# Optimization experiments

Hardware: AMD Instinct MI355X
Metric: run time of the kernel (lower is better)

## Reference

```python
import jax, jax.numpy as jnp
import numpy as np
from jax import lax

UP = 4          # upscale_factor (pixel_shuffle factor hardcoded to 4 in ReconBlock)
OUT_CH = UP * UP * 5 * 5  # 400
MID_CH = UP * 5           # 20


def setup_inputs() -> dict:
    key = jax.random.key(0)
    ks = jax.random.split(key, 5)
    B, A, H, W = 2, 5, 96, 96
    pic = jax.random.uniform(ks[0], (B, A, A, H, W), dtype=jnp.float32)
    w1 = jax.random.normal(ks[1], (OUT_CH, 1, 5, 5, 9, 9), dtype=jnp.float32) * 0.02
    b1 = jnp.zeros((OUT_CH,), jnp.float32)
    w2a = jax.random.normal(ks[2], (MID_CH, 1, 3, 3, 5, 5), dtype=jnp.float32) * 0.02
    b2a = jnp.zeros((MID_CH,), jnp.float32)
    w2b = jax.random.normal(ks[3], (OUT_CH, MID_CH, 3, 3, 5, 5), dtype=jnp.float32) * 0.02
    b2b = jnp.zeros((OUT_CH,), jnp.float32)
    return {"pic": pic, "w1": w1, "b1": b1, "w2a": w2a, "b2a": b2a,
            "w2b": w2b, "b2b": b2b}


def _conv4d(x, w):
    # x: [B, Cin, A1, A2, H, W], w: [Cout, Cin, k1, k2, k3, k4], VALID, stride 1
    return lax.conv_general_dilated(x, w, window_strides=(1, 1, 1, 1),
                                    padding='VALID')


def _bias(b):
    return b[None, :, None, None, None, None]


def reference(pic, w1, b1, w2a, b2a, w2b, b2b):
    B, A1, A2, H, W = pic.shape
    # Padder: pad H,W by 4 each side with value 0.5
    padded = jnp.full((B, A1, A2, H + 8, W + 8), 0.5, dtype=pic.dtype)
    padded = padded.at[:, :, :, 4:-4, 4:-4].set(pic)
    x = padded[:, None]  # [B,1,A1,A2,H+8,W+8]

    # DimBlock_1: single 4D conv (5,5,9,9); ReLU defined but never applied
    p1 = _conv4d(x, w1) + _bias(b1)              # [B,400,1,1,H,W]

    # DimBlock_2: two 4D convs (3,3,5,5) with ReLU
    buf = jax.nn.relu(_conv4d(x, w2a) + _bias(b2a))   # [B,20,3,3,H+4,W+4]
    p2 = jax.nn.relu(_conv4d(buf, w2b) + _bias(b2b))  # [B,400,1,1,H,W]

    # BottleNeck
    mid = (p1 + p2) / 2                           # [B,400,1,1,H,W]

    # ReconBlock: take angular position (0,0), pixel_shuffle(4), split 25 -> 5x5
    y = mid[:, :, 0, 0]                           # [B,400,H,W]
    Bc, C, Hh, Ww = y.shape
    r = 4
    y = y.reshape(Bc, 25, r, r, Hh, Ww)
    y = y.transpose(0, 1, 4, 2, 5, 3).reshape(Bc, 25, Hh * r, Ww * r)
    return y.reshape(Bc, 5, 5, Hh * r, Ww * r)
```

## Files before the change

kernel.cpp:

```cpp
#include <hip/hip_runtime.h>
#include <hip/hip_bf16.h>


typedef __attribute__((ext_vector_type(8))) unsigned short ushort8;
typedef __attribute__((ext_vector_type(8))) __bf16 bf16x8;
typedef __attribute__((ext_vector_type(4))) float f32x4;

#define NB 2
#define HSLOT 576
#define WST 14336

static __device__ __forceinline__ unsigned short f2bf(float f) {
    __hip_bfloat16 h = __float2bfloat16(f);
    return *reinterpret_cast<unsigned short*>(&h);
}
static __device__ __forceinline__ float bf2f(unsigned short u) {
    unsigned int v = ((unsigned int)u) << 16;
    return __uint_as_float(v);
}
static __device__ __forceinline__ void gload16(const unsigned short* g, unsigned short* l) {
    __builtin_amdgcn_global_load_lds(
        (const __attribute__((address_space(1))) unsigned int*)(const void*)g,
        (__attribute__((address_space(3))) unsigned int*)(void*)l, 16, 0, 0);
}

__global__ __launch_bounds__(256) void pad_kernel(const float* __restrict__ pic,
                                                  unsigned short* __restrict__ Pn,
                                                  unsigned short* __restrict__ Pp) {
    int idx = blockIdx.x * 256 + threadIdx.x;
    if (idx >= NB * 104 * 104) return;
    int x = idx % 104;
    int y = (idx / 104) % 104;
    int b = idx / (104 * 104);
    unsigned short vals[32];
    bool inter = (y >= 4 && y < 100 && x >= 4 && x < 100);
#pragma unroll
    for (int c = 0; c < 25; ++c) {
        float v = inter ? pic[((b * 25 + c) * 96 + (y - 4)) * 96 + (x - 4)] : 0.5f;
        vals[c] = f2bf(v);
        Pp[((b * 25 + c) * 104 + y) * 104 + x] = vals[c];
    }
#pragma unroll
    for (int c = 25; c < 32; ++c) vals[c] = 0;
    ushort8* dst = (ushort8*)(Pn + idx * 32);
#pragma unroll
    for (int j = 0; j < 4; ++j) dst[j] = *(ushort8*)&vals[j * 8];
}

#define NWA (6 * 25 * 7 * 4 * 64 * 8)
#define NWB (81 * 7 * 4 * 64 * 8)
__global__ __launch_bounds__(256) void prep_w_kernel(const float* __restrict__ w2b,
                                                     const float* __restrict__ w1,
                                                     unsigned short* __restrict__ WpA,
                                                     unsigned short* __restrict__ WpB) {
    int idx = blockIdx.x * 256 + threadIdx.x;
    if (idx < NWA) {
        int e = idx & 7, lane = (idx >> 3) & 63, n = (idx >> 9) & 3;
        int r = idx >> 11;
        int ocb = r % 7; r /= 7;
        int tap = r % 25; int cc = r / 25;
        int oc = ocb * 64 + n * 16 + (lane & 15);
        int k  = cc * 32 + (lane >> 4) * 8 + e;
        float v = 0.f;
        if (oc < 400 && k < 180) {
            int mc = k % 20, uv = k / 20;
            v = w2b[oc * 4500 + (mc * 9 + uv) * 25 + tap];
        }
        WpA[idx] = f2bf(v);
    } else {
        int kx = idx - NWA;
        if (kx >= NWB) return;
        int e = kx & 7, lane = (kx >> 3) & 63, n = (kx >> 9) & 3;
        int r = kx >> 11;
        int ocb = r % 7; int tp = r / 7;
        int dy, dx;
        if (tp < 45) { dy = tp / 5; dx = tp % 5; }
        else { int u = tp - 45; dy = u >> 2; dx = 5 + (u & 3); }
        int oc = ocb * 64 + n * 16 + (lane & 15);
        int c  = (lane >> 4) * 8 + e;
        float v = (oc < 400 && c < 25) ? w1[oc * 2025 + c * 81 + (dy * 9 + dx)] : 0.f;
        WpB[kx] = f2bf(v);
    }
}

__global__ __launch_bounds__(256) void conv2a_kernel(const unsigned short* __restrict__ Pp,
                                                     const float* __restrict__ w2a,
                                                     const float* __restrict__ b2a,
                                                     unsigned short* __restrict__ Bn) {
    __shared__ float sIn[9 * 20 * 21];
    __shared__ float sW[20 * 225];
    const int b   = blockIdx.z;
    const int uv  = blockIdx.y;
    const int u   = uv / 3, v = uv % 3;
    const int tx0 = (blockIdx.x % 7) * 16;
    const int ty0 = (blockIdx.x / 7) * 16;
    const int tid = threadIdx.x;

    for (int i = tid; i < 20 * 225; i += 256) sW[i] = w2a[i];
    for (int i = tid; i < 9 * 20 * 20; i += 256) {
        int ch9 = i / 400;
        int r   = (i / 20) % 20;
        int cl  = i % 20;
        int c   = (u + ch9 / 3) * 5 + (v + ch9 % 3);
        int gy  = min(ty0 + r, 103);
        int gx  = min(tx0 + cl, 103);
        sIn[ch9 * 420 + r * 21 + cl] = bf2f(Pp[((b * 25 + c) * 104 + gy) * 104 + gx]);
    }
    __syncthreads();

    const int mcg = tid >> 6;
    const int pid = tid & 63;
    const int px  = (pid & 7) * 2;
    const int py  = (pid >> 3) * 2;

    float acc[5][2][2];
#pragma unroll
    for (int m = 0; m < 5; m++)
#pragma unroll
        for (int r = 0; r < 2; r++)
#pragma unroll
            for (int c = 0; c < 2; c++) acc[m][r][c] = 0.f;

    for (int ch9 = 0; ch9 < 9; ++ch9) {
        const float* in = &sIn[ch9 * 420];
#pragma unroll
        for (int dy = 0; dy < 5; ++dy) {
            float ra[6], rb[6];
#pragma unroll
            for (int k = 0; k < 6; k++) {
                ra[k] = in[(py + dy) * 21 + px + k];
                rb[k] = in[(py + 1 + dy) * 21 + px + k];
            }
#pragma unroll
            for (int dx = 0; dx < 5; ++dx) {
#pragma unroll
                for (int m = 0; m < 5; m++) {
                    float wv = sW[(mcg * 5 + m) * 225 + ch9 * 25 + dy * 5 + dx];
                    acc[m][0][0] += ra[dx] * wv;
                    acc[m][0][1] += ra[dx + 1] * wv;
                    acc[m][1][0] += rb[dx] * wv;
                    acc[m][1][1] += rb[dx + 1] * wv;
                }
            }
        }
    }

#pragma unroll
    for (int m = 0; m < 5; m++) {
        int mc = mcg * 5 + m;
        float bias = b2a[mc];
        int gp = uv * 20 + mc;
#pragma unroll
        for (int r = 0; r < 2; r++) {
            int y = ty0 + py + r;
            if (y >= 100) continue;
#pragma unroll
            for (int c = 0; c < 2; c++) {
                int x = tx0 + px + c;
                if (x >= 100) continue;
                Bn[((b * 100 + y) * 100 + x) * 192 + gp] = f2bf(fmaxf(acc[m][r][c] + bias, 0.f));
                if (uv == 0 && mcg == 3) {
#pragma unroll
                    for (int z = 0; z < 12; ++z)
                        Bn[((b * 100 + y) * 100 + x) * 192 + 180 + z] = 0;
                }
            }
        }
    }
}

#define MFMA16(A0, A1, A2, A3, B0, B1, B2, B3)                                          \
    {                                                                                   \
        __builtin_amdgcn_s_setprio(1);                                                  \
        acc[0][0] = __builtin_amdgcn_mfma_f32_16x16x32_bf16(A0, B0, acc[0][0], 0, 0, 0);\
        acc[0][1] = __builtin_amdgcn_mfma_f32_16x16x32_bf16(A0, B1, acc[0][1], 0, 0, 0);\
        acc[0][2] = __builtin_amdgcn_mfma_f32_16x16x32_bf16(A0, B2, acc[0][2], 0, 0, 0);\
        acc[0][3] = __builtin_amdgcn_mfma_f32_16x16x32_bf16(A0, B3, acc[0][3], 0, 0, 0);\
        acc[1][0] = __builtin_amdgcn_mfma_f32_16x16x32_bf16(A1, B0, acc[1][0], 0, 0, 0);\
        acc[1][1] = __builtin_amdgcn_mfma_f32_16x16x32_bf16(A1, B1, acc[1][1], 0, 0, 0);\
        acc[1][2] = __builtin_amdgcn_mfma_f32_16x16x32_bf16(A1, B2, acc[1][2], 0, 0, 0);\
        acc[1][3] = __builtin_amdgcn_mfma_f32_16x16x32_bf16(A1, B3, acc[1][3], 0, 0, 0);\
        acc[2][0] = __builtin_amdgcn_mfma_f32_16x16x32_bf16(A2, B0, acc[2][0], 0, 0, 0);\
        acc[2][1] = __builtin_amdgcn_mfma_f32_16x16x32_bf16(A2, B1, acc[2][1], 0, 0, 0);\
        acc[2][2] = __builtin_amdgcn_mfma_f32_16x16x32_bf16(A2, B2, acc[2][2], 0, 0, 0);\
        acc[2][3] = __builtin_amdgcn_mfma_f32_16x16x32_bf16(A2, B3, acc[2][3], 0, 0, 0);\
        acc[3][0] = __builtin_amdgcn_mfma_f32_16x16x32_bf16(A3, B0, acc[3][0], 0, 0, 0);\
        acc[3][1] = __builtin_amdgcn_mfma_f32_16x16x32_bf16(A3, B1, acc[3][1], 0, 0, 0);\
        acc[3][2] = __builtin_amdgcn_mfma_f32_16x16x32_bf16(A3, B2, acc[3][2], 0, 0, 0);\
        acc[3][3] = __builtin_amdgcn_mfma_f32_16x16x32_bf16(A3, B3, acc[3][3], 0, 0, 0);\
        __builtin_amdgcn_s_setprio(0);                                                  \
    }

__global__ __launch_bounds__(256, 2) void conv_mfma_kernel(
    const unsigned short* __restrict__ Pn, const unsigned short* __restrict__ Bn,
    const unsigned short* __restrict__ WpA, const unsigned short* __restrict__ WpB,
    const float* __restrict__ b1, const float* __restrict__ b2b,
    float* __restrict__ out) {
    __shared__ __align__(16) unsigned short sHalo[4 * HSLOT * 8];

    const int tid  = threadIdx.x;
    const int lane = tid & 63, w = tid >> 6;
    const int l15  = lane & 15, lhi = lane >> 4;
    const int ocB  = blockIdx.y;
    const int pb   = blockIdx.x;
    const int b    = pb / 36;
    const int t36  = pb % 36;
    const int ty0  = (t36 / 3) * 8;
    const int tx0  = (t36 % 3) * 32;

    const int vA = (lhi * HSLOT + w * 72 + l15) * 8;

    float bb2[4], bb1[4];
#pragma unroll
    for (int n = 0; n < 4; ++n) {
        int oc  = ocB * 64 + n * 16 + l15;
        int occ = oc < 400 ? oc : 399;
        bb2[n] = b2b[occ];
        bb1[n] = b1[occ];
    }

    f32x4 acc[4][4] = {};

    auto stage_halo = [&](int seg) {
        if (seg < 6) {
            for (int L2 = 0; L2 < 7; ++L2) {
                int p = L2 * 64 + lane;
                if (p >= 432) p = 0;
                int hy = (p * 58255) >> 21;
                int hx = p - hy * 36;
                gload16(Bn + ((size_t)((b * 100 + ty0 + hy) * 100 + tx0 + hx)) * 192 +
                            seg * 32 + w * 8,
                        &sHalo[(w * HSLOT + L2 * 64) * 8]);
            }
        } else {
            int cx = tx0 + (seg == 7 ? 5 : 0);
            for (int L2 = 0; L2 < 9; ++L2) {
                int p = L2 * 64 + lane;
                int hy = (p * 58255) >> 21;
                int hx = p - hy * 36;
                int gx = cx + hx;
                gx = gx > 103 ? 103 : gx;
                gload16(Pn + ((size_t)((b * 104 + ty0 + hy) * 104 + gx)) * 32 + w * 8,
                        &sHalo[(w * HSLOT + L2 * 64) * 8]);
            }
        }
    };

    auto computeA = [&](int cc) {
        const unsigned short* wp = WpA + ((size_t)(cc * 25 * 7 + ocB)) * 2048 + lane * 8;
        bf16x8 c0 = *(const bf16x8*)(wp);
        bf16x8 c1 = *(const bf16x8*)(wp + 512);
        bf16x8 c2 = *(const bf16x8*)(wp + 1024);
        bf16x8 c3 = *(const bf16x8*)(wp + 1536);
        for (int dy = 0; dy < 5; ++dy) {
            const unsigned short* ha = &sHalo[vA + dy * 288];
#pragma unroll
            for (int dx = 0; dx < 5; ++dx) {
                wp += WST;
                bf16x8 n0 = *(const bf16x8*)(wp);
                bf16x8 n1 = *(const bf16x8*)(wp + 512);
                bf16x8 n2 = *(const bf16x8*)(wp + 1024);
                bf16x8 n3 = *(const bf16x8*)(wp + 1536);
                bf16x8 a0 = *(const bf16x8*)&ha[dx * 8];
                bf16x8 a1 = *(const bf16x8*)&ha[dx * 8 + 128];
                bf16x8 a2 = *(const bf16x8*)&ha[dx * 8 + 288];
                bf16x8 a3 = *(const bf16x8*)&ha[dx * 8 + 416];
                MFMA16(a0, a1, a2, a3, c0, c1, c2, c3);
                c0 = n0; c1 = n1; c2 = n2; c3 = n3;
            }
        }
    };

    auto computeB1 = [&]() {
        const unsigned short* wp = WpB + (size_t)ocB * 2048 + lane * 8;
        bf16x8 c0 = *(const bf16x8*)(wp);
        bf16x8 c1 = *(const bf16x8*)(wp + 512);
        bf16x8 c2 = *(const bf16x8*)(wp + 1024);
        bf16x8 c3 = *(const bf16x8*)(wp + 1536);
        for (int dy = 0; dy < 9; ++dy) {
            const unsigned short* ha = &sHalo[vA + dy * 288];
#pragma unroll
            for (int dx = 0; dx < 5; ++dx) {
                wp += WST;
                bf16x8 n0 = *(const bf16x8*)(wp);
                bf16x8 n1 = *(const bf16x8*)(wp + 512);
                bf16x8 n2 = *(const bf16x8*)(wp + 1024);
                bf16x8 n3 = *(const bf16x8*)(wp + 1536);
                bf16x8 a0 = *(const bf16x8*)&ha[dx * 8];
                bf16x8 a1 = *(const bf16x8*)&ha[dx * 8 + 128];
                bf16x8 a2 = *(const bf16x8*)&ha[dx * 8 + 288];
                bf16x8 a3 = *(const bf16x8*)&ha[dx * 8 + 416];
                MFMA16(a0, a1, a2, a3, c0, c1, c2, c3);
                c0 = n0; c1 = n1; c2 = n2; c3 = n3;
            }
        }
    };

    auto computeB2 = [&]() {
        const unsigned short* wp = WpB + (size_t)(45 * 7 + ocB) * 2048 + lane * 8;
        bf16x8 c0 = *(const bf16x8*)(wp);
        bf16x8 c1 = *(const bf16x8*)(wp + 512);
        bf16x8 c2 = *(const bf16x8*)(wp + 1024);
        bf16x8 c3 = *(const bf16x8*)(wp + 1536);
        for (int dy = 0; dy < 9; ++dy) {
            const unsigned short* ha = &sHalo[vA + dy * 288];
#pragma unroll
            for (int dxl = 0; dxl < 4; ++dxl) {
                wp += WST;
                bf16x8 n0 = c0, n1 = c1, n2 = c2, n3 = c3;
                if (dy < 8 || dxl < 3) {
                    n0 = *(const bf16x8*)(wp);
                    n1 = *(const bf16x8*)(wp + 512);
                    n2 = *(const bf16x8*)(wp + 1024);
                    n3 = *(const bf16x8*)(wp + 1536);
                }
                bf16x8 a0 = *(const bf16x8*)&ha[dxl * 8];
                bf16x8 a1 = *(const bf16x8*)&ha[dxl * 8 + 128];
                bf16x8 a2 = *(const bf16x8*)&ha[dxl * 8 + 288];
                bf16x8 a3 = *(const bf16x8*)&ha[dxl * 8 + 416];
                MFMA16(a0, a1, a2, a3, c0, c1, c2, c3);
                c0 = n0; c1 = n1; c2 = n2; c3 = n3;
            }
        }
    };

    stage_halo(0);
    __syncthreads();
    computeA(0);
    for (int cc = 1; cc < 6; ++cc) {
        __syncthreads();
        stage_halo(cc);
        __syncthreads();
        computeA(cc);
    }

    __syncthreads();
    stage_halo(6);
#pragma unroll
    for (int m = 0; m < 4; ++m)
#pragma unroll
        for (int n = 0; n < 4; ++n)
#pragma unroll
            for (int i = 0; i < 4; ++i)
                acc[m][n][i] = fmaxf(acc[m][n][i] + bb2[n], 0.f);
    __syncthreads();
    computeB1();

    __syncthreads();
    stage_halo(7);
    __syncthreads();
    computeB2();

#pragma unroll
    for (int n = 0; n < 4; ++n) {
        int oc = ocB * 64 + n * 16 + l15;
        if (oc >= 400) continue;
        float bv = bb1[n];
        int c25 = oc >> 4, r1 = (oc >> 2) & 3, r2 = oc & 3;
#pragma unroll
        for (int m = 0; m < 4; ++m) {
            int y  = ty0 + w * 2 + (m >> 1);
            int x0 = tx0 + (m & 1) * 16 + lhi * 4;
#pragma unroll
            for (int i = 0; i < 4; ++i) {
                out[((size_t)(b * 25 + c25) * 384 + y * 4 + r1) * 384 + (x0 + i) * 4 + r2] =
                    (acc[m][n][i] + bv) * 0.5f;
            }
        }
    }
}

extern "C" void kernel_launch(void* const* d_in, const int* in_sizes, int n_in,
                              void* d_out, int out_size, void* d_ws, size_t ws_size,
                              hipStream_t stream) {
    const float* pic = (const float*)d_in[0];
    const float* w1  = (const float*)d_in[1];
    const float* b1  = (const float*)d_in[2];
    const float* w2a = (const float*)d_in[3];
    const float* b2a = (const float*)d_in[4];
    const float* w2b = (const float*)d_in[5];
    const float* b2b = (const float*)d_in[6];
    float* out = (float*)d_out;

    char* ws = (char*)d_ws;
    unsigned short* Pn  = (unsigned short*)(ws);
    unsigned short* Bn  = (unsigned short*)(ws + 1384448);
    unsigned short* WpA = (unsigned short*)(ws + 9064448);
    unsigned short* WpB = (unsigned short*)(ws + 13365248);
    unsigned short* Pp  = WpA;

    pad_kernel<<<(NB * 104 * 104 + 255) / 256, 256, 0, stream>>>(pic, Pn, Pp);
    conv2a_kernel<<<dim3(49, 9, NB), 256, 0, stream>>>(Pp, w2a, b2a, Bn);
    prep_w_kernel<<<(NWA + NWB + 255) / 256, 256, 0, stream>>>(w2b, w1, WpA, WpB);
    conv_mfma_kernel<<<dim3(72, 7), 256, 0, stream>>>(Pn, Bn, WpA, WpB, b1, b2b, out);
}
```

Baseline: 171.7 us.

## Move conv2a to MFMA and double-buffer halo staging in main conv

The scalar FP32 first-stage convolution becomes an MFMA kernel. It builds a banded weight matrix over the 25 angular channels in LDS and reads the channel-packed padded input directly, so the planar padded copy is no longer needed. In the main conv kernel, halo staging is double-buffered: the next segment's global-to-LDS load is issued before the current segment's MFMAs, and the full syncthreads pairs are replaced with a vmcnt wait plus a barrier. The loops are flattened with register prefetch of the A fragments. This aims to cut conv2a compute time and hide load latency, at the cost of doubled LDS use in the main kernel, which may reduce occupancy.

```diff
diff --git a/kernel.cpp b/kernel.cpp
--- a/kernel.cpp
+++ b/kernel.cpp
@@ -8,165 +8,19 @@
 
 #define NB 2
 #define HSLOT 576
+#define HBUF (4 * HSLOT * 8)
 #define WST 14336
+#define NWA (6 * 25 * 7 * 4 * 64 * 8)
+#define NWB (81 * 7 * 4 * 64 * 8)
 
 static __device__ __forceinline__ unsigned short f2bf(float f) {
     __hip_bfloat16 h = __float2bfloat16(f);
     return *reinterpret_cast<unsigned short*>(&h);
-}
-static __device__ __forceinline__ float bf2f(unsigned short u) {
-    unsigned int v = ((unsigned int)u) << 16;
-    return __uint_as_float(v);
 }
 static __device__ __forceinline__ void gload16(const unsigned short* g, unsigned short* l) {
     __builtin_amdgcn_global_load_lds(
         (const __attribute__((address_space(1))) unsigned int*)(const void*)g,
         (__attribute__((address_space(3))) unsigned int*)(void*)l, 16, 0, 0);
-}
-
-__global__ __launch_bounds__(256) void pad_kernel(const float* __restrict__ pic,
-                                                  unsigned short* __restrict__ Pn,
-                                                  unsigned short* __restrict__ Pp) {
-    int idx = blockIdx.x * 256 + threadIdx.x;
-    if (idx >= NB * 104 * 104) return;
-    int x = idx % 104;
-    int y = (idx / 104) % 104;
-    int b = idx / (104 * 104);
-    unsigned short vals[32];
-    bool inter = (y >= 4 && y < 100 && x >= 4 && x < 100);
-#pragma unroll
-    for (int c = 0; c < 25; ++c) {
-        float v = inter ? pic[((b * 25 + c) * 96 + (y - 4)) * 96 + (x - 4)] : 0.5f;
-        vals[c] = f2bf(v);
-        Pp[((b * 25 + c) * 104 + y) * 104 + x] = vals[c];
-    }
-#pragma unroll
-    for (int c = 25; c < 32; ++c) vals[c] = 0;
-    ushort8* dst = (ushort8*)(Pn + idx * 32);
-#pragma unroll
-    for (int j = 0; j < 4; ++j) dst[j] = *(ushort8*)&vals[j * 8];
-}
-
-#define NWA (6 * 25 * 7 * 4 * 64 * 8)
-#define NWB (81 * 7 * 4 * 64 * 8)
-__global__ __launch_bounds__(256) void prep_w_kernel(const float* __restrict__ w2b,
-                                                     const float* __restrict__ w1,
-                                                     unsigned short* __restrict__ WpA,
-                                                     unsigned short* __restrict__ WpB) {
-    int idx = blockIdx.x * 256 + threadIdx.x;
-    if (idx < NWA) {
-        int e = idx & 7, lane = (idx >> 3) & 63, n = (idx >> 9) & 3;
-        int r = idx >> 11;
-        int ocb = r % 7; r /= 7;
-        int tap = r % 25; int cc = r / 25;
-        int oc = ocb * 64 + n * 16 + (lane & 15);
-        int k  = cc * 32 + (lane >> 4) * 8 + e;
-        float v = 0.f;
-        if (oc < 400 && k < 180) {
-            int mc = k % 20, uv = k / 20;
-            v = w2b[oc * 4500 + (mc * 9 + uv) * 25 + tap];
-        }
-        WpA[idx] = f2bf(v);
-    } else {
-        int kx = idx - NWA;
-        if (kx >= NWB) return;
-        int e = kx & 7, lane = (kx >> 3) & 63, n = (kx >> 9) & 3;
-        int r = kx >> 11;
-        int ocb = r % 7; int tp = r / 7;
-        int dy, dx;
-        if (tp < 45) { dy = tp / 5; dx = tp % 5; }
-        else { int u = tp - 45; dy = u >> 2; dx = 5 + (u & 3); }
-        int oc = ocb * 64 + n * 16 + (lane & 15);
-        int c  = (lane >> 4) * 8 + e;
-        float v = (oc < 400 && c < 25) ? w1[oc * 2025 + c * 81 + (dy * 9 + dx)] : 0.f;
-        WpB[kx] = f2bf(v);
-    }
-}
-
-__global__ __launch_bounds__(256) void conv2a_kernel(const unsigned short* __restrict__ Pp,
-                                                     const float* __restrict__ w2a,
-                                                     const float* __restrict__ b2a,
-                                                     unsigned short* __restrict__ Bn) {
-    __shared__ float sIn[9 * 20 * 21];
-    __shared__ float sW[20 * 225];
-    const int b   = blockIdx.z;
-    const int uv  = blockIdx.y;
-    const int u   = uv / 3, v = uv % 3;
-    const int tx0 = (blockIdx.x % 7) * 16;
-    const int ty0 = (blockIdx.x / 7) * 16;
-    const int tid = threadIdx.x;
-
-    for (int i = tid; i < 20 * 225; i += 256) sW[i] = w2a[i];
-    for (int i = tid; i < 9 * 20 * 20; i += 256) {
-        int ch9 = i / 400;
-        int r   = (i / 20) % 20;
-        int cl  = i % 20;
-        int c   = (u + ch9 / 3) * 5 + (v + ch9 % 3);
-        int gy  = min(ty0 + r, 103);
-        int gx  = min(tx0 + cl, 103);
-        sIn[ch9 * 420 + r * 21 + cl] = bf2f(Pp[((b * 25 + c) * 104 + gy) * 104 + gx]);
-    }
-    __syncthreads();
-
-    const int mcg = tid >> 6;
-    const int pid = tid & 63;
-    const int px  = (pid & 7) * 2;
-    const int py  = (pid >> 3) * 2;
-
-    float acc[5][2][2];
-#pragma unroll
-    for (int m = 0; m < 5; m++)
-#pragma unroll
-        for (int r = 0; r < 2; r++)
-#pragma unroll
-            for (int c = 0; c < 2; c++) acc[m][r][c] = 0.f;
-
-    for (int ch9 = 0; ch9 < 9; ++ch9) {
-        const float* in = &sIn[ch9 * 420];
-#pragma unroll
-        for (int dy = 0; dy < 5; ++dy) {
-            float ra[6], rb[6];
-#pragma unroll
-            for (int k = 0; k < 6; k++) {
-                ra[k] = in[(py + dy) * 21 + px + k];
-                rb[k] = in[(py + 1 + dy) * 21 + px + k];
-            }
-#pragma unroll
-            for (int dx = 0; dx < 5; ++dx) {
-#pragma unroll
-                for (int m = 0; m < 5; m++) {
-                    float wv = sW[(mcg * 5 + m) * 225 + ch9 * 25 + dy * 5 + dx];
-                    acc[m][0][0] += ra[dx] * wv;
-                    acc[m][0][1] += ra[dx + 1] * wv;
-                    acc[m][1][0] += rb[dx] * wv;
-                    acc[m][1][1] += rb[dx + 1] * wv;
-                }
-            }
-        }
-    }
-
-#pragma unroll
-    for (int m = 0; m < 5; m++) {
-        int mc = mcg * 5 + m;
-        float bias = b2a[mc];
-        int gp = uv * 20 + mc;
-#pragma unroll
-        for (int r = 0; r < 2; r++) {
-            int y = ty0 + py + r;
-            if (y >= 100) continue;
-#pragma unroll
-            for (int c = 0; c < 2; c++) {
-                int x = tx0 + px + c;
-                if (x >= 100) continue;
-                Bn[((b * 100 + y) * 100 + x) * 192 + gp] = f2bf(fmaxf(acc[m][r][c] + bias, 0.f));
-                if (uv == 0 && mcg == 3) {
-#pragma unroll
-                    for (int z = 0; z < 12; ++z)
-                        Bn[((b * 100 + y) * 100 + x) * 192 + 180 + z] = 0;
-                }
-            }
-        }
-    }
 }
 
 #define MFMA16(A0, A1, A2, A3, B0, B1, B2, B3)                                          \
@@ -191,12 +45,168 @@
         __builtin_amdgcn_s_setprio(0);                                                  \
     }
 
+__global__ __launch_bounds__(256) void pad_kernel(const float* __restrict__ pic,
+                                                  unsigned short* __restrict__ Pn) {
+    int idx = blockIdx.x * 256 + threadIdx.x;
+    if (idx >= NB * 104 * 104) return;
+    int x = idx % 104;
+    int y = (idx / 104) % 104;
+    int b = idx / (104 * 104);
+    unsigned short vals[32];
+    bool inter = (y >= 4 && y < 100 && x >= 4 && x < 100);
+#pragma unroll
+    for (int c = 0; c < 25; ++c) {
+        float v = inter ? pic[((b * 25 + c) * 96 + (y - 4)) * 96 + (x - 4)] : 0.5f;
+        vals[c] = f2bf(v);
+    }
+#pragma unroll
+    for (int c = 25; c < 32; ++c) vals[c] = 0;
+    ushort8* dst = (ushort8*)(Pn + idx * 32);
+#pragma unroll
+    for (int j = 0; j < 4; ++j) dst[j] = *(ushort8*)&vals[j * 8];
+}
+
+__global__ __launch_bounds__(256) void prep_w_kernel(const float* __restrict__ w2b,
+                                                     const float* __restrict__ w1,
+                                                     unsigned short* __restrict__ Wp) {
+    int idx = blockIdx.x * 256 + threadIdx.x;
+    if (idx < NWA) {
+        int e = idx & 7, lane = (idx >> 3) & 63, n = (idx >> 9) & 3;
+        int r = idx >> 11;
+        int ocb = r % 7; r /= 7;
+        int tap = r % 25; int cc = r / 25;
+        int oc = ocb * 64 + n * 16 + (lane & 15);
+        int k  = cc * 32 + (lane >> 4) * 8 + e;
+        float v = 0.f;
+        if (oc < 400 && k < 180) {
+            int mc = k % 20, uv = k / 20;
+            v = w2b[oc * 4500 + (mc * 9 + uv) * 25 + tap];
+        }
+        Wp[idx] = f2bf(v);
+    } else {
+        int kx = idx - NWA;
+        if (kx >= NWB) return;
+        int e = kx & 7, lane = (kx >> 3) & 63, n = (kx >> 9) & 3;
+        int r = kx >> 11;
+        int ocb = r % 7; int tp = r / 7;
+        int dy, dx;
+        if (tp < 45) { dy = tp / 5; dx = tp % 5; }
+        else { int u = tp - 45; dy = u >> 2; dx = 5 + (u & 3); }
+        int oc = ocb * 64 + n * 16 + (lane & 15);
+        int c  = (lane >> 4) * 8 + e;
+        float v = (oc < 400 && c < 25) ? w1[oc * 2025 + c * 81 + (dy * 9 + dx)] : 0.f;
+        Wp[NWA + kx] = f2bf(v);
+    }
+}
+
+__global__ __launch_bounds__(256) void conv2a_mfma_kernel(
+    const unsigned short* __restrict__ Pn, const float* __restrict__ w2a,
+    const float* __restrict__ b2a, unsigned short* __restrict__ Bn) {
+    __shared__ __align__(16) unsigned short sWc[25 * 2048];
+    __shared__ __align__(16) unsigned short sHalo[4 * 448 * 8];
+
+    const int tid  = threadIdx.x;
+    const int lane = tid & 63, w = tid >> 6;
+    const int l15  = lane & 15, lhi = lane >> 4;
+    const int gx0  = blockIdx.x;
+    const int b    = gx0 / 52, t52 = gx0 % 52;
+    const int ty0  = (t52 >> 2) * 8;
+    const int tx0  = (t52 & 3) * 32;
+    const int ocB  = blockIdx.y;
+
+    {
+        int oc = ocB * 64 + w * 16 + (lane & 15);
+        int kb = (lane >> 4) * 8;
+        int uv = oc / 20;
+        int mc = oc - uv * 20;
+        int u = uv / 3, v = uv - (uv / 3) * 3;
+        const float* wb[8];
+#pragma unroll
+        for (int e = 0; e < 8; ++e) {
+            int k  = kb + e;
+            int c1 = k / 5, c2 = k - (k / 5) * 5;
+            int da1 = c1 - u, da2 = c2 - v;
+            bool valid = (oc < 180) && ((unsigned)da1 < 3u) && ((unsigned)da2 < 3u);
+            wb[e] = valid ? (w2a + mc * 225 + (da1 * 3 + da2) * 25) : (const float*)0;
+        }
+#pragma unroll
+        for (int tap = 0; tap < 25; ++tap) {
+            unsigned short fr[8];
+#pragma unroll
+            for (int e = 0; e < 8; ++e) fr[e] = wb[e] ? f2bf(wb[e][tap]) : (unsigned short)0;
+            *(ushort8*)&sWc[tap * 2048 + tid * 8] = *(ushort8*)fr;
+        }
+    }
+
+    for (int L2 = 0; L2 < 7; ++L2) {
+        int p = L2 * 64 + lane;
+        if (p >= 432) p = 0;
+        int hy = (p * 58255) >> 21, hx = p - hy * 36;
+        int gy = ty0 + hy; gy = gy > 103 ? 103 : gy;
+        int gx = tx0 + hx; gx = gx > 103 ? 103 : gx;
+        gload16(Pn + ((size_t)((b * 104 + gy) * 104 + gx)) * 32 + w * 8,
+                &sHalo[(w * 448 + L2 * 64) * 8]);
+    }
+    float bs[4];
+#pragma unroll
+    for (int n = 0; n < 4; ++n) {
+        int oc = ocB * 64 + n * 16 + l15;
+        bs[n] = (oc < 180) ? b2a[oc % 20] : 0.f;
+    }
+    __syncthreads();
+
+    const unsigned short* hb = &sHalo[(lhi * 448 + w * 72 + l15) * 8];
+    const unsigned short* wc = &sWc[lane * 8];
+
+    f32x4 acc[4][4] = {};
+    bf16x8 a0 = *(const bf16x8*)(hb), a1 = *(const bf16x8*)(hb + 128);
+    bf16x8 a2 = *(const bf16x8*)(hb + 288), a3 = *(const bf16x8*)(hb + 416);
+    bf16x8 c0 = *(const bf16x8*)(wc), c1 = *(const bf16x8*)(wc + 512);
+    bf16x8 c2 = *(const bf16x8*)(wc + 1024), c3 = *(const bf16x8*)(wc + 1536);
+    bf16x8 q0, q1, q2, q3, n0, n1, n2, n3;
+#pragma unroll
+    for (int t = 0; t < 25; ++t) {
+        if (t < 24) {
+            const int u = (((t + 1) / 5) * 36 + ((t + 1) % 5)) * 8;
+            q0 = *(const bf16x8*)(hb + u);
+            q1 = *(const bf16x8*)(hb + u + 128);
+            q2 = *(const bf16x8*)(hb + u + 288);
+            q3 = *(const bf16x8*)(hb + u + 416);
+            const unsigned short* wn = wc + (t + 1) * 2048;
+            n0 = *(const bf16x8*)(wn);
+            n1 = *(const bf16x8*)(wn + 512);
+            n2 = *(const bf16x8*)(wn + 1024);
+            n3 = *(const bf16x8*)(wn + 1536);
+        }
+        MFMA16(a0, a1, a2, a3, c0, c1, c2, c3);
+        if (t < 24) { a0 = q0; a1 = q1; a2 = q2; a3 = q3;
+                      c0 = n0; c1 = n1; c2 = n2; c3 = n3; }
+    }
+
+#pragma unroll
+    for (int n = 0; n < 4; ++n) {
+        int oc = ocB * 64 + n * 16 + l15;
+#pragma unroll
+        for (int m = 0; m < 4; ++m) {
+            int y = ty0 + w * 2 + (m >> 1);
+            if (y >= 100) continue;
+            int x0 = tx0 + (m & 1) * 16 + lhi * 4;
+#pragma unroll
+            for (int i = 0; i < 4; ++i) {
+                int x = x0 + i;
+                if (x >= 100) continue;
+                Bn[((size_t)((b * 100 + y) * 100 + x)) * 192 + oc] =
+                    f2bf(fmaxf(acc[m][n][i] + bs[n], 0.f));
+            }
+        }
+    }
+}
+
 __global__ __launch_bounds__(256, 2) void conv_mfma_kernel(
     const unsigned short* __restrict__ Pn, const unsigned short* __restrict__ Bn,
-    const unsigned short* __restrict__ WpA, const unsigned short* __restrict__ WpB,
-    const float* __restrict__ b1, const float* __restrict__ b2b,
-    float* __restrict__ out) {
-    __shared__ __align__(16) unsigned short sHalo[4 * HSLOT * 8];
+    const unsigned short* __restrict__ Wp, const float* __restrict__ b1,
+    const float* __restrict__ b2b, float* __restrict__ out) {
+    __shared__ __align__(16) unsigned short sHalo[2 * HBUF];
 
     const int tid  = threadIdx.x;
     const int lane = tid & 63, w = tid >> 6;
@@ -210,6 +220,30 @@
 
     const int vA = (lhi * HSLOT + w * 72 + l15) * 8;
 
+    auto stageA = [&](int cc, int par) {
+        unsigned short* dst0 = &sHalo[par * HBUF + w * HSLOT * 8];
+        for (int L2 = 0; L2 < 7; ++L2) {
+            int p = L2 * 64 + lane;
+            if (p >= 432) p = 0;
+            int hy = (p * 58255) >> 21, hx = p - hy * 36;
+            gload16(Bn + ((size_t)((b * 100 + ty0 + hy) * 100 + tx0 + hx)) * 192 +
+                        cc * 32 + w * 8,
+                    dst0 + L2 * 512);
+        }
+    };
+    auto stageB = [&](int seg, int par) {
+        int cx = tx0 + (seg == 7 ? 5 : 0);
+        unsigned short* dst0 = &sHalo[par * HBUF + w * HSLOT * 8];
+        for (int L2 = 0; L2 < 9; ++L2) {
+            int p = L2 * 64 + lane;
+            int hy = (p * 58255) >> 21, hx = p - hy * 36;
+            int gx = cx + hx;
+            gx = gx > 103 ? 103 : gx;
+            gload16(Pn + ((size_t)((b * 104 + ty0 + hy) * 104 + gx)) * 32 + w * 8,
+                    dst0 + L2 * 512);
+        }
+    };
+
     float bb2[4], bb1[4];
 #pragma unroll
     for (int n = 0; n < 4; ++n) {
@@ -219,137 +253,110 @@
         bb1[n] = b1[occ];
     }
 
+    const unsigned short* wq = Wp + ocB * 2048 + lane * 8;
+    bf16x8 c0 = *(const bf16x8*)(wq);
+    bf16x8 c1 = *(const bf16x8*)(wq + 512);
+    bf16x8 c2 = *(const bf16x8*)(wq + 1024);
+    bf16x8 c3 = *(const bf16x8*)(wq + 1536);
+    stageA(0, 0);
+    __syncthreads();
+
     f32x4 acc[4][4] = {};
-
-    auto stage_halo = [&](int seg) {
-        if (seg < 6) {
-            for (int L2 = 0; L2 < 7; ++L2) {
-                int p = L2 * 64 + lane;
-                if (p >= 432) p = 0;
-                int hy = (p * 58255) >> 21;
-                int hx = p - hy * 36;
-                gload16(Bn + ((size_t)((b * 100 + ty0 + hy) * 100 + tx0 + hx)) * 192 +
-                            seg * 32 + w * 8,
-                        &sHalo[(w * HSLOT + L2 * 64) * 8]);
+    bf16x8 a0, a1, a2, a3, q0, q1, q2, q3, n0, n1, n2, n3;
+
+    for (int cc = 0; cc < 6; ++cc) {
+        const unsigned short* hb = &sHalo[(cc & 1) * HBUF + vA];
+        a0 = *(const bf16x8*)(hb);
+        a1 = *(const bf16x8*)(hb + 128);
+        a2 = *(const bf16x8*)(hb + 288);
+        a3 = *(const bf16x8*)(hb + 416);
+        if (cc < 5) stageA(cc + 1, (cc + 1) & 1);
+        else        stageB(6, 0);
+#pragma unroll
+        for (int t = 0; t < 25; ++t) {
+            wq += WST;
+            n0 = *(const bf16x8*)(wq);
+            n1 = *(const bf16x8*)(wq + 512);
+            n2 = *(const bf16x8*)(wq + 1024);
+            n3 = *(const bf16x8*)(wq + 1536);
+            if (t < 24) {
+                const int u = (((t + 1) / 5) * 36 + ((t + 1) % 5)) * 8;
+                q0 = *(const bf16x8*)(hb + u);
+                q1 = *(const bf16x8*)(hb + u + 128);
+                q2 = *(const bf16x8*)(hb + u + 288);
+                q3 = *(const bf16x8*)(hb + u + 416);
             }
-        } else {
-            int cx = tx0 + (seg == 7 ? 5 : 0);
-            for (int L2 = 0; L2 < 9; ++L2) {
-                int p = L2 * 64 + lane;
-                int hy = (p * 58255) >> 21;
-                int hx = p - hy * 36;
-                int gx = cx + hx;
-                gx = gx > 103 ? 103 : gx;
-                gload16(Pn + ((size_t)((b * 104 + ty0 + hy) * 104 + gx)) * 32 + w * 8,
-                        &sHalo[(w * HSLOT + L2 * 64) * 8]);
+            MFMA16(a0, a1, a2, a3, c0, c1, c2, c3);
+            c0 = n0; c1 = n1; c2 = n2; c3 = n3;
+            if (t < 24) { a0 = q0; a1 = q1; a2 = q2; a3 = q3; }
+        }
+        if (cc == 5) {
+#pragma unroll
+            for (int m = 0; m < 4; ++m)
+#pragma unroll
+                for (int n = 0; n < 4; ++n)
+#pragma unroll
+                    for (int i = 0; i < 4; ++i)
+                        acc[m][n][i] = fmaxf(acc[m][n][i] + bb2[n], 0.f);
+        }
+        asm volatile("s_waitcnt vmcnt(4)" ::: "memory");
+        asm volatile("s_barrier" ::: "memory");
+    }
+
+    {
+        const unsigned short* hb = &sHalo[vA];
+        a0 = *(const bf16x8*)(hb);
+        a1 = *(const bf16x8*)(hb + 128);
+        a2 = *(const bf16x8*)(hb + 288);
+        a3 = *(const bf16x8*)(hb + 416);
+        stageB(7, 1);
+#pragma unroll
+        for (int t = 0; t < 45; ++t) {
+            wq += WST;
+            n0 = *(const bf16x8*)(wq);
+            n1 = *(const bf16x8*)(wq + 512);
+            n2 = *(const bf16x8*)(wq + 1024);
+            n3 = *(const bf16x8*)(wq + 1536);
+            if (t < 44) {
+                const int u = (((t + 1) / 5) * 36 + ((t + 1) % 5)) * 8;
+                q0 = *(const bf16x8*)(hb + u);
+                q1 = *(const bf16x8*)(hb + u + 128);
+                q2 = *(const bf16x8*)(hb + u + 288);
+                q3 = *(const bf16x8*)(hb + u + 416);
             }
-        }
-    };
-
-    auto computeA = [&](int cc) {
-        const unsigned short* wp = WpA + ((size_t)(cc * 25 * 7 + ocB)) * 2048 + lane * 8;
-        bf16x8 c0 = *(const bf16x8*)(wp);
-        bf16x8 c1 = *(const bf16x8*)(wp + 512);
-        bf16x8 c2 = *(const bf16x8*)(wp + 1024);
-        bf16x8 c3 = *(const bf16x8*)(wp + 1536);
-        for (int dy = 0; dy < 5; ++dy) {
-            const unsigned short* ha = &sHalo[vA + dy * 288];
-#pragma unroll
-            for (int dx = 0; dx < 5; ++dx) {
-                wp += WST;
-                bf16x8 n0 = *(const bf16x8*)(wp);
-                bf16x8 n1 = *(const bf16x8*)(wp + 512);
-                bf16x8 n2 = *(const bf16x8*)(wp + 1024);
-                bf16x8 n3 = *(const bf16x8*)(wp + 1536);
-                bf16x8 a0 = *(const bf16x8*)&ha[dx * 8];
-                bf16x8 a1 = *(const bf16x8*)&ha[dx * 8 + 128];
-                bf16x8 a2 = *(const bf16x8*)&ha[dx * 8 + 288];
-                bf16x8 a3 = *(const bf16x8*)&ha[dx * 8 + 416];
-                MFMA16(a0, a1, a2, a3, c0, c1, c2, c3);
-                c0 = n0; c1 = n1; c2 = n2; c3 = n3;
+            MFMA16(a0, a1, a2, a3, c0, c1, c2, c3);
+            c0 = n0; c1 = n1; c2 = n2; c3 = n3;
+            if (t < 44) { a0 = q0; a1 = q1; a2 = q2; a3 = q3; }
+        }
+        asm volatile("s_waitcnt vmcnt(4)" ::: "memory");
+        asm volatile("s_barrier" ::: "memory");
+    }
+
+    {
+        const unsigned short* hb = &sHalo[HBUF + vA];
+        a0 = *(const bf16x8*)(hb);
+        a1 = *(const bf16x8*)(hb + 128);
+        a2 = *(const bf16x8*)(hb + 288);
+        a3 = *(const bf16x8*)(hb + 416);
+#pragma unroll
+        for (int t = 0; t < 36; ++t) {
+            if (t < 35) {
+                wq += WST;
+                n0 = *(const bf16x8*)(wq);
+                n1 = *(const bf16x8*)(wq + 512);
+                n2 = *(const bf16x8*)(wq + 1024);
+                n3 = *(const bf16x8*)(wq + 1536);
+                const int u = (((t + 1) / 4) * 36 + ((t + 1) % 4)) * 8;
+                q0 = *(const bf16x8*)(hb + u);
+                q1 = *(const bf16x8*)(hb + u + 128);
+                q2 = *(const bf16x8*)(hb + u + 288);
+                q3 = *(const bf16x8*)(hb + u + 416);
             }
-        }
-    };
-
-    auto computeB1 = [&]() {
-        const unsigned short* wp = WpB + (size_t)ocB * 2048 + lane * 8;
-        bf16x8 c0 = *(const bf16x8*)(wp);
-        bf16x8 c1 = *(const bf16x8*)(wp + 512);
-        bf16x8 c2 = *(const bf16x8*)(wp + 1024);
-        bf16x8 c3 = *(const bf16x8*)(wp + 1536);
-        for (int dy = 0; dy < 9; ++dy) {
-            const unsigned short* ha = &sHalo[vA + dy * 288];
-#pragma unroll
-            for (int dx = 0; dx < 5; ++dx) {
-                wp += WST;
-                bf16x8 n0 = *(const bf16x8*)(wp);
-                bf16x8 n1 = *(const bf16x8*)(wp + 512);
-                bf16x8 n2 = *(const bf16x8*)(wp + 1024);
-                bf16x8 n3 = *(const bf16x8*)(wp + 1536);
-                bf16x8 a0 = *(const bf16x8*)&ha[dx * 8];
-                bf16x8 a1 = *(const bf16x8*)&ha[dx * 8 + 128];
-                bf16x8 a2 = *(const bf16x8*)&ha[dx * 8 + 288];
-                bf16x8 a3 = *(const bf16x8*)&ha[dx * 8 + 416];
-                MFMA16(a0, a1, a2, a3, c0, c1, c2, c3);
-                c0 = n0; c1 = n1; c2 = n2; c3 = n3;
-            }
-        }
-    };
-
-    auto computeB2 = [&]() {
-        const unsigned short* wp = WpB + (size_t)(45 * 7 + ocB) * 2048 + lane * 8;
-        bf16x8 c0 = *(const bf16x8*)(wp);
-        bf16x8 c1 = *(const bf16x8*)(wp + 512);
-        bf16x8 c2 = *(const bf16x8*)(wp + 1024);
-        bf16x8 c3 = *(const bf16x8*)(wp + 1536);
-        for (int dy = 0; dy < 9; ++dy) {
-            const unsigned short* ha = &sHalo[vA + dy * 288];
-#pragma unroll
-            for (int dxl = 0; dxl < 4; ++dxl) {
-                wp += WST;
-                bf16x8 n0 = c0, n1 = c1, n2 = c2, n3 = c3;
-                if (dy < 8 || dxl < 3) {
-                    n0 = *(const bf16x8*)(wp);
-                    n1 = *(const bf16x8*)(wp + 512);
-                    n2 = *(const bf16x8*)(wp + 1024);
-                    n3 = *(const bf16x8*)(wp + 1536);
-                }
-                bf16x8 a0 = *(const bf16x8*)&ha[dxl * 8];
-                bf16x8 a1 = *(const bf16x8*)&ha[dxl * 8 + 128];
-                bf16x8 a2 = *(const bf16x8*)&ha[dxl * 8 + 288];
-                bf16x8 a3 = *(const bf16x8*)&ha[dxl * 8 + 416];
-                MFMA16(a0, a1, a2, a3, c0, c1, c2, c3);
-                c0 = n0; c1 = n1; c2 = n2; c3 = n3;
-            }
-        }
-    };
-
-    stage_halo(0);
-    __syncthreads();
-    computeA(0);
-    for (int cc = 1; cc < 6; ++cc) {
-        __syncthreads();
-        stage_halo(cc);
-        __syncthreads();
-        computeA(cc);
-    }
-
-    __syncthreads();
-    stage_halo(6);
-#pragma unroll
-    for (int m = 0; m < 4; ++m)
-#pragma unroll
-        for (int n = 0; n < 4; ++n)
-#pragma unroll
-            for (int i = 0; i < 4; ++i)
-                acc[m][n][i] = fmaxf(acc[m][n][i] + bb2[n], 0.f);
-    __syncthreads();
-    computeB1();
-
-    __syncthreads();
-    stage_halo(7);
-    __syncthreads();
-    computeB2();
+            MFMA16(a0, a1, a2, a3, c0, c1, c2, c3);
+            if (t < 35) { a0 = q0; a1 = q1; a2 = q2; a3 = q3;
+                          c0 = n0; c1 = n1; c2 = n2; c3 = n3; }
+        }
+    }
 
 #pragma unroll
     for (int n = 0; n < 4; ++n) {
@@ -383,14 +390,12 @@
     float* out = (float*)d_out;
 
     char* ws = (char*)d_ws;
-    unsigned short* Pn  = (unsigned short*)(ws);
-    unsigned short* Bn  = (unsigned short*)(ws + 1384448);
-    unsigned short* WpA = (unsigned short*)(ws + 9064448);
-    unsigned short* WpB = (unsigned short*)(ws + 13365248);
-    unsigned short* Pp  = WpA;
-
-    pad_kernel<<<(NB * 104 * 104 + 255) / 256, 256, 0, stream>>>(pic, Pn, Pp);
-    conv2a_kernel<<<dim3(49, 9, NB), 256, 0, stream>>>(Pp, w2a, b2a, Bn);
-    prep_w_kernel<<<(NWA + NWB + 255) / 256, 256, 0, stream>>>(w2b, w1, WpA, WpB);
-    conv_mfma_kernel<<<dim3(72, 7), 256, 0, stream>>>(Pn, Bn, WpA, WpB, b1, b2b, out);
-}
+    unsigned short* Pn = (unsigned short*)(ws);
+    unsigned short* Bn = (unsigned short*)(ws + 1384448);
+    unsigned short* Wp = (unsigned short*)(ws + 9064448);
+
+    pad_kernel<<<(NB * 104 * 104 + 255) / 256, 256, 0, stream>>>(pic, Pn);
+    prep_w_kernel<<<(NWA + NWB + 255) / 256, 256, 0, stream>>>(w2b, w1, Wp);
+    conv2a_mfma_kernel<<<dim3(104, 3), 256, 0, stream>>>(Pn, w2a, b2a, Bn);
+    conv_mfma_kernel<<<dim3(72, 7), 256, 0, stream>>>(Pn, Bn, Wp, b1, b2b, out);
+}
```

After: 160.0 us (median of 2 runs). -6.8%, faster.
